# Kernel tuning notes

Hardware: AMD Instinct MI355X
Metric: run time of the kernel (lower is better)

The kernel has to match this reference:

```python
import jax, jax.numpy as jnp
import numpy as np

C = 32          # d_model / channels
D_STATE = 32
D_CONV = 4
EXPAND = 2
D_INNER = EXPAND * C          # 64
DT_RANK = (C + 15) // 16      # ceil(32/16) = 2
EPS = 1e-5


def _conv2d(x, w, b):
    # x: (B,C,H,W), w: (O,I,3,3), stride 1, padding 1 (torch Conv2d)
    y = jax.lax.conv_general_dilated(
        x, w, window_strides=(1, 1), padding=[(1, 1), (1, 1)],
        dimension_numbers=("NCHW", "OIHW", "NCHW"))
    return y + b[None, :, None, None]


def _silu(x):
    return x * jax.nn.sigmoid(x)


def _mamba(xs, in_proj_w, conv1d_w, conv1d_b, x_proj_w, dt_proj_w, dt_proj_b,
           A_log, Dp, out_proj_w):
    # xs: (B, L, C)
    xz = xs @ in_proj_w.T                       # (B, L, 2*D_INNER)
    xm, z = jnp.split(xz, 2, axis=-1)           # each (B, L, D_INNER)

    # causal depthwise conv1d along L (torch: padding=d_conv-1 then [..., :L])
    xc = xm.transpose(0, 2, 1)                  # (B, D_INNER, L)
    xc = jax.lax.conv_general_dilated(
        xc, conv1d_w, window_strides=(1,), padding=[(D_CONV - 1, 0)],
        dimension_numbers=("NCH", "OIH", "NCH"),
        feature_group_count=D_INNER)
    xm = _silu((xc + conv1d_b[None, :, None]).transpose(0, 2, 1))  # (B,L,D_INNER)

    x_dbl = xm @ x_proj_w.T                     # (B, L, DT_RANK + 2*D_STATE)
    dt = x_dbl[..., :DT_RANK]
    Bm = x_dbl[..., DT_RANK:DT_RANK + D_STATE]  # (B, L, N)
    Cm = x_dbl[..., DT_RANK + D_STATE:]         # (B, L, N)

    delta = jax.nn.softplus(dt @ dt_proj_w.T + dt_proj_b)  # (B, L, D_INNER)
    A = -jnp.exp(A_log)                                     # (D_INNER, N)

    deltaA = jnp.exp(delta[..., None] * A)                           # (B,L,D,N)
    deltaBx = delta[..., None] * Bm[:, :, None, :] * xm[..., None]   # (B,L,D,N)

    def combine(c1, c2):
        a1, b1 = c1
        a2, b2 = c2
        return a1 * a2, a2 * b1 + b2

    # parallel linear recurrence h_t = deltaA_t * h_{t-1} + deltaBx_t
    _, hstate = jax.lax.associative_scan(combine, (deltaA, deltaBx), axis=1)

    y = jnp.einsum("bldn,bln->bld", hstate, Cm) + xm * Dp
    y = y * _silu(z)
    return y @ out_proj_w.T                     # (B, L, C)


def setup_inputs() -> dict:
    key = jax.random.key(0)
    ks = jax.random.split(key, 16)
    s = 0.02
    inp = {
        "x": jax.random.normal(ks[0], (4, C, 64, 64), dtype=jnp.float32),
        "conv1_w": jax.random.normal(ks[1], (2 * C, C, 3, 3), jnp.float32) * s,
        "conv1_b": jnp.zeros((2 * C,), jnp.float32),
        "conv2_w": jax.random.normal(ks[2], (C, 2 * C, 3, 3), jnp.float32) * s,
        "conv2_b": jnp.zeros((C,), jnp.float32),
        "ln_g": jnp.ones((C,), jnp.float32),
        "ln_b": jnp.zeros((C,), jnp.float32),
        "in_proj_w": jax.random.normal(ks[3], (2 * D_INNER, C), jnp.float32) * s,
        "conv1d_w": jax.random.normal(ks[4], (D_INNER, 1, D_CONV), jnp.float32) * 0.1,
        "conv1d_b": jnp.zeros((D_INNER,), jnp.float32),
        "x_proj_w": jax.random.normal(ks[5], (DT_RANK + 2 * D_STATE, D_INNER), jnp.float32) * s,
        "dt_proj_w": jax.random.normal(ks[6], (D_INNER, DT_RANK), jnp.float32) * 0.1,
        "dt_proj_b": jax.random.normal(ks[7], (D_INNER,), jnp.float32) * 0.1 - 4.0,
        "A_log": jnp.log(jnp.tile(jnp.arange(1, D_STATE + 1, dtype=jnp.float32), (D_INNER, 1))),
        "Dp": jnp.ones((D_INNER,), jnp.float32),
        "out_proj_w": jax.random.normal(ks[8], (C, D_INNER), jnp.float32) * s,
        "smooth_w": jax.random.normal(ks[9], (C, C, 3, 3), jnp.float32) * s,
        "smooth_b": jnp.zeros((C,), jnp.float32),
    }
    return inp


def reference(x, conv1_w, conv1_b, conv2_w, conv2_b, ln_g, ln_b,
              in_proj_w, conv1d_w, conv1d_b, x_proj_w, dt_proj_w, dt_proj_b,
              A_log, Dp, out_proj_w, smooth_w, smooth_b):
    b, c, h, w = x.shape
    # convb residual
    t = jax.nn.relu(_conv2d(x, conv1_w, conv1_b))
    x = _conv2d(t, conv2_w, conv2_b) + x
    # reshape (b,c,h,w) -> (b, h*w, c) row-major (faithful to torch .reshape)
    xs = x.reshape(b, -1, c)
    # LayerNorm over last dim
    mu = jnp.mean(xs, axis=-1, keepdims=True)
    var = jnp.mean(jnp.square(xs - mu), axis=-1, keepdims=True)
    xs = (xs - mu) * jax.lax.rsqrt(var + EPS) * ln_g + ln_b
    # Mamba block
    y = _mamba(xs, in_proj_w, conv1d_w, conv1d_b, x_proj_w, dt_proj_w,
               dt_proj_b, A_log, Dp, out_proj_w)
    y = y.transpose(0, 2, 1).reshape(b, c, h, w)
    return _conv2d(y, smooth_w, smooth_b)
```

## Files before the change

### kernel.cpp

```cpp
#include <hip/hip_runtime.h>
#include <math.h>

#define SEQL 4096
#define L2E 1.44269504088896340736f

#if defined(__has_builtin)
#if __has_builtin(__builtin_amdgcn_exp2f)
#define FAST_EXP2(x) __builtin_amdgcn_exp2f(x)
#endif
#endif
#ifndef FAST_EXP2
#define FAST_EXP2(x) exp2f(x)
#endif

__device__ __forceinline__ float sigmoid_f(float x){ return 1.0f/(1.0f+expf(-x)); }

template<int CI, int CO, int COG, bool RELU, bool RES>
__global__ __launch_bounds__(256) void conv3x3_k(const float* __restrict__ in,
    const float* __restrict__ wgt, const float* __restrict__ bias,
    const float* __restrict__ res, float* __restrict__ out)
{
  constexpr int CIT = CI/4;
  __shared__ float tin[4][2][6][72];
  __shared__ float red[3][4][COG][66];
  const int tid  = threadIdx.x;
  const int lane = tid & 63;
  const int ty   = tid >> 6;
  const int h0   = blockIdx.x * 4;
  const int co0  = blockIdx.y * COG;
  const int b    = blockIdx.z;

  if (lane < 24){
    int cl = lane / 12, rem = lane % 12, r = rem >> 1, side = rem & 1;
    tin[ty][cl][r][side ? 68 : 3] = 0.0f;
  }

  float acc[4][COG];
  #pragma unroll
  for (int rr=0;rr<4;++rr)
    #pragma unroll
    for (int u=0;u<COG;++u) acc[rr][u] = 0.0f;

  const int ci0 = ty*CIT;
  for (int cig = ci0; cig < ci0 + CIT; cig += 2){
    #pragma unroll
    for (int k=0;k<3;++k){
      int idx4 = lane + (k<<6);
      int row  = idx4 >> 4;
      int cl = row/6, r = row - cl*6;
      int w4 = (idx4 & 15) << 2;
      int h  = h0 - 1 + r;
      float4 v = make_float4(0.f,0.f,0.f,0.f);
      if (h>=0 && h<64)
        v = *(const float4*)(in + ((size_t)(b*CI+cig+cl)*64 + h)*64 + w4);
      *(float4*)&tin[ty][cl][r][4+w4] = v;
    }
    #pragma unroll
    for (int cl=0; cl<2; ++cl){
      float rv[6][3];
      #pragma unroll
      for (int r=0;r<6;++r)
        #pragma unroll
        for (int c=0;c<3;++c)
          rv[r][c] = tin[ty][cl][r][3+lane+c];
      #pragma unroll
      for (int u=0;u<COG;++u){
        const float* wp = wgt + ((size_t)(co0+u)*CI + cig + cl)*9;
        #pragma unroll
        for (int rr=0;rr<4;++rr)
          #pragma unroll
          for (int j=0;j<3;++j){
            acc[rr][u] = fmaf(rv[rr+j][0], wp[3*j+0], acc[rr][u]);
            acc[rr][u] = fmaf(rv[rr+j][1], wp[3*j+1], acc[rr][u]);
            acc[rr][u] = fmaf(rv[rr+j][2], wp[3*j+2], acc[rr][u]);
          }
      }
    }
  }
  if (ty > 0){
    #pragma unroll
    for (int rr=0;rr<4;++rr)
      #pragma unroll
      for (int u=0;u<COG;++u) red[ty-1][rr][u][lane] = acc[rr][u];
  }
  __syncthreads();
  if (ty == 0){
    #pragma unroll
    for (int rr=0;rr<4;++rr)
      #pragma unroll
      for (int u=0;u<COG;++u){
        float s = acc[rr][u] + red[0][rr][u][lane] + red[1][rr][u][lane]
                + red[2][rr][u][lane] + bias[co0+u];
        size_t ob = ((size_t)(b*CO+co0+u)*64 + h0+rr)*64 + lane;
        if constexpr (RES)  s += res[ob];
        if constexpr (RELU) s = fmaxf(s, 0.0f);
        out[ob] = s;
      }
  }
}

__global__ __launch_bounds__(512) void mamba_in_k(const float* __restrict__ x2,
    const float* __restrict__ g, const float* __restrict__ be,
    const float* __restrict__ Wip, const float* __restrict__ cw,
    const float* __restrict__ cb, const float* __restrict__ Wxp,
    const float* __restrict__ Wdt, const float* __restrict__ bdt,
    const float* __restrict__ A_log,
    float* __restrict__ xm2, float* __restrict__ szb, float* __restrict__ dlt,
    float* __restrict__ Bm, float* __restrict__ Cm,
    float* __restrict__ cA, float* __restrict__ cH)
{
  __shared__ float xn[68][37];
  __shared__ float xm[64][68];
  __shared__ float xt[64][67];
  __shared__ float xd[64][67];
  const int tid = threadIdx.x, lane = tid & 63, ty = tid >> 6;
  const int bi = blockIdx.x >> 6;
  const int l0 = (blockIdx.x & 63) << 6;

  if (ty < 2){
    int t = ty*64 + lane;
    if (t < 67){
      int tok = l0 - 3 + t;
      if (tok >= 0){
        const float* row = x2 + (size_t)bi*131072 + (size_t)tok*32;
        float v[32];
        #pragma unroll
        for (int c=0;c<32;c+=4){
          float4 f = *(const float4*)(row + c);
          v[c]=f.x; v[c+1]=f.y; v[c+2]=f.z; v[c+3]=f.w;
        }
        float p[8];
        #pragma unroll
        for (int j2=0;j2<8;++j2) p[j2]=v[j2];
        #pragma unroll
        for (int i=8;i<32;i+=8){
          #pragma unroll
          for (int j2=0;j2<8;++j2) p[j2]+=v[i+j2];
        }
        float mu = (((p[0]+p[1])+(p[2]+p[3]))+((p[4]+p[5])+(p[6]+p[7]))) * 0.03125f;
        float q[8];
        #pragma unroll
        for (int j2=0;j2<8;++j2){ float dd=v[j2]-mu; q[j2]=dd*dd; }
        #pragma unroll
        for (int i=8;i<32;i+=8){
          #pragma unroll
          for (int j2=0;j2<8;++j2){ float dd=v[i+j2]-mu; q[j2]+=dd*dd; }
        }
        float var = (((q[0]+q[1])+(q[2]+q[3]))+((q[4]+q[5])+(q[6]+q[7]))) * 0.03125f;
        float rstd = 1.0f / sqrtf(var + 1e-5f);
        #pragma unroll
        for (int c=0;c<32;++c) xn[t][c] = (v[c]-mu)*rstd*g[c] + be[c];
      } else {
        #pragma unroll
        for (int c=0;c<32;++c) xn[t][c] = 0.0f;
      }
    }
  }
  __syncthreads();

  const int d0 = ty*8;
  {
    float xvA[32];
    #pragma unroll
    for (int c=0;c<32;++c) xvA[c] = xn[lane][c];
    #pragma unroll
    for (int jj=0;jj<8;++jj){
      const float* wr = Wip + (d0+jj)*32;
      float a = 0.0f;
      #pragma unroll
      for (int c=0;c<32;++c) a = fmaf(xvA[c], wr[c], a);
      xm[d0+jj][lane] = a;
    }
  }
  if (lane < 3){
    float xvB[32];
    #pragma unroll
    for (int c=0;c<32;++c) xvB[c] = xn[64+lane][c];
    #pragma unroll
    for (int jj=0;jj<8;++jj){
      const float* wr = Wip + (d0+jj)*32;
      float a = 0.0f;
      #pragma unroll
      for (int c=0;c<32;++c) a = fmaf(xvB[c], wr[c], a);
      xm[d0+jj][64+lane] = a;
    }
  }
  {
    float xvC[32];
    #pragma unroll
    for (int c=0;c<32;++c) xvC[c] = xn[lane+3][c];
    #pragma unroll
    for (int jj=0;jj<8;++jj){
      const float* wr = Wip + (64+d0+jj)*32;
      float a = 0.0f;
      #pragma unroll
      for (int c=0;c<32;++c) a = fmaf(xvC[c], wr[c], a);
      szb[((size_t)(bi*64+d0+jj))*SEQL + l0 + lane] = a * sigmoid_f(a);
    }
  }
  __syncthreads();

  #pragma unroll
  for (int jj=0;jj<8;++jj){
    int d = d0 + jj;
    float a = xm[d][lane]*cw[d*4] + xm[d][lane+1]*cw[d*4+1]
            + xm[d][lane+2]*cw[d*4+2] + xm[d][lane+3]*cw[d*4+3] + cb[d];
    float s = a * sigmoid_f(a);
    xt[lane][d] = s;
    xm2[((size_t)(bi*64+d))*SEQL + l0 + lane] = s;
  }
  __syncthreads();

  {
    float xv[64];
    #pragma unroll
    for (int c=0;c<64;++c) xv[c] = xt[lane][c];
    for (int j=ty; j<66; j+=8){
      const float* wr = Wxp + j*64;
      float a = 0.0f;
      #pragma unroll
      for (int c=0;c<64;++c) a = fmaf(xv[c], wr[c], a);
      xd[lane][j] = a;
    }
  }
  __syncthreads();

  {
    float dt0 = xd[lane][0], dt1 = xd[lane][1];
    #pragma unroll
    for (int k=0;k<8;++k){
      int d2 = ty*8 + k;
      float v = dt0*Wdt[d2*2] + dt1*Wdt[d2*2+1] + bdt[d2];
      float sp = fmaxf(v,0.0f) + log1pf(expf(-fabsf(v)));
      dlt[((size_t)(bi*64+d2))*SEQL + l0 + lane] = sp;
      xm[d2][lane] = sp;
    }
    const int which = ty >> 2, gq = ty & 3;
    float* dst = which ? Cm : Bm;
    size_t base = ((size_t)bi*SEQL + l0 + lane)*32 + gq*8;
    const int s0 = 2 + which*32 + gq*8;
    float4 f0, f1;
    f0.x = xd[lane][s0+0]; f0.y = xd[lane][s0+1]; f0.z = xd[lane][s0+2]; f0.w = xd[lane][s0+3];
    f1.x = xd[lane][s0+4]; f1.y = xd[lane][s0+5]; f1.z = xd[lane][s0+6]; f1.w = xd[lane][s0+7];
    *(float4*)(dst + base)     = f0;
    *(float4*)(dst + base + 4) = f1;
  }
  __syncthreads();

  {
    const int d  = tid >> 3;
    const int gg = tid & 7;
    const int chunk = blockIdx.x & 63;
    const int bd = bi*64 + d;
    float Av2[4], h[4] = {0,0,0,0}, aP[4] = {1,1,1,1};
    #pragma unroll
    for (int j=0;j<4;++j) Av2[j] = -expf(A_log[d*32 + gg + 8*j]) * L2E;
    #pragma unroll 4
    for (int t=0;t<64;++t){
      float dlv = xm[d][t];
      float xv2 = xt[t][d];
      #pragma unroll
      for (int j=0;j<4;++j){
        float bv = xd[t][2 + gg + 8*j];
        float a = FAST_EXP2(dlv*Av2[j]);
        h[j] = fmaf(a, h[j], dlv*bv*xv2);
        aP[j] *= a;
      }
    }
    #pragma unroll
    for (int j=0;j<4;++j){
      size_t idx = (((size_t)bd<<5) + gg + 8*j)*64 + chunk;
      cA[idx] = aP[j]; cH[idx] = h[j];
    }
  }
}

__global__ __launch_bounds__(256) void scan_p2(const float* __restrict__ dlt,
    const float* __restrict__ xssm, const float* __restrict__ Bm,
    const float* __restrict__ Cm, const float* __restrict__ A_log,
    const float* __restrict__ Dp, const float* __restrict__ sz,
    const float* __restrict__ cA, const float* __restrict__ cHs,
    float* __restrict__ yt)
{
  __shared__ float pre[32][9];
  const int tid = threadIdx.x;
  const int n = tid & 31;
  const int grp = blockIdx.x & 7;
  const int chunk = grp*8 + (tid >> 5);
  const int bd = blockIdx.x >> 3;
  const int b = bd >> 6, d = bd & 63;
  const int l0 = chunk << 6;

  if (tid < 32){
    const float* pa = cA  + (((size_t)bd<<5)+tid)*64;
    const float* ph = cHs + (((size_t)bd<<5)+tid)*64;
    float hrun = 0.0f;
    for (int c=0;c<grp*8;c+=4){
      float4 a4 = *(const float4*)(pa+c);
      float4 h4 = *(const float4*)(ph+c);
      hrun = fmaf(a4.x,hrun,h4.x);
      hrun = fmaf(a4.y,hrun,h4.y);
      hrun = fmaf(a4.z,hrun,h4.z);
      hrun = fmaf(a4.w,hrun,h4.w);
    }
    int c = grp*8;
    float4 a4 = *(const float4*)(pa+c);
    float4 h4 = *(const float4*)(ph+c);
    pre[tid][0]=hrun; hrun=fmaf(a4.x,hrun,h4.x);
    pre[tid][1]=hrun; hrun=fmaf(a4.y,hrun,h4.y);
    pre[tid][2]=hrun; hrun=fmaf(a4.z,hrun,h4.z);
    pre[tid][3]=hrun; hrun=fmaf(a4.w,hrun,h4.w);
    a4 = *(const float4*)(pa+c+4);
    h4 = *(const float4*)(ph+c+4);
    pre[tid][4]=hrun; hrun=fmaf(a4.x,hrun,h4.x);
    pre[tid][5]=hrun; hrun=fmaf(a4.y,hrun,h4.y);
    pre[tid][6]=hrun; hrun=fmaf(a4.z,hrun,h4.z);
    pre[tid][7]=hrun;
  }
  __syncthreads();

  const float Av2 = -expf(A_log[d*32+n]) * L2E;
  const float Dv = Dp[d];
  const float* del = dlt  + (size_t)bd*SEQL + l0;
  const float* xp  = xssm + (size_t)bd*SEQL + l0;
  const float* szp = sz   + (size_t)bd*SEQL + l0;
  const float* Bp  = Bm + ((size_t)b*SEQL + l0)*32 + n;
  const float* Cp  = Cm + ((size_t)b*SEQL + l0)*32 + n;
  float* yp = yt + (size_t)bd*SEQL + l0;
  float h = pre[n][tid >> 5];
  #pragma unroll 2
  for (int i0=0;i0<64;i0+=4){
    float4 d4 = *(const float4*)(del+i0);
    float4 x4 = *(const float4*)(xp +i0);
    float4 s4 = *(const float4*)(szp+i0);
    float b0 = Bp[(i0+0)*32], b1 = Bp[(i0+1)*32], b2 = Bp[(i0+2)*32], b3 = Bp[(i0+3)*32];
    float c0 = Cp[(i0+0)*32], c1 = Cp[(i0+1)*32], c2 = Cp[(i0+2)*32], c3 = Cp[(i0+3)*32];
    float a0 = FAST_EXP2(d4.x*Av2); h = fmaf(a0,h, d4.x*b0*x4.x);
    float v0 = h*c0;
    float a1 = FAST_EXP2(d4.y*Av2); h = fmaf(a1,h, d4.y*b1*x4.y);
    float v1 = h*c1;
    float a2 = FAST_EXP2(d4.z*Av2); h = fmaf(a2,h, d4.z*b2*x4.z);
    float v2 = h*c2;
    float a3 = FAST_EXP2(d4.w*Av2); h = fmaf(a3,h, d4.w*b3*x4.w);
    float v3 = h*c3;
    v0 += __shfl_xor(v0,16); v0 += __shfl_xor(v0,8); v0 += __shfl_xor(v0,4);
    v0 += __shfl_xor(v0,2);  v0 += __shfl_xor(v0,1);
    v1 += __shfl_xor(v1,16); v1 += __shfl_xor(v1,8); v1 += __shfl_xor(v1,4);
    v1 += __shfl_xor(v1,2);  v1 += __shfl_xor(v1,1);
    v2 += __shfl_xor(v2,16); v2 += __shfl_xor(v2,8); v2 += __shfl_xor(v2,4);
    v2 += __shfl_xor(v2,2);  v2 += __shfl_xor(v2,1);
    v3 += __shfl_xor(v3,16); v3 += __shfl_xor(v3,8); v3 += __shfl_xor(v3,4);
    v3 += __shfl_xor(v3,2);  v3 += __shfl_xor(v3,1);
    if (n==0){
      yp[i0+0] = fmaf(x4.x, Dv, v0) * s4.x;
      yp[i0+1] = fmaf(x4.y, Dv, v1) * s4.y;
      yp[i0+2] = fmaf(x4.z, Dv, v2) * s4.z;
      yp[i0+3] = fmaf(x4.w, Dv, v3) * s4.w;
    }
  }
}

__global__ __launch_bounds__(512) void outproj_k(const float* __restrict__ yt,
    const float* __restrict__ Wout, float* __restrict__ ym)
{
  __shared__ float ys[64][67];
  const int tid = threadIdx.x, lane = tid & 63, ty = tid >> 6;
  const int bi = blockIdx.x >> 6;
  const int l0 = (blockIdx.x & 63) << 6;
  for (int r=ty; r<64; r+=8)
    ys[lane][r] = yt[((size_t)(bi*64+r))*SEQL + l0 + lane];
  __syncthreads();
  float yv[64];
  #pragma unroll
  for (int c=0;c<64;++c) yv[c] = ys[lane][c];
  #pragma unroll
  for (int jj=0;jj<4;++jj){
    int j = ty*4 + jj;
    const float* wr = Wout + j*64;
    float acc = 0.0f;
    #pragma unroll
    for (int c=0;c<64;++c) acc = fmaf(yv[c], wr[c], acc);
    ym[((size_t)(bi*32+j))*SEQL + l0 + lane] = acc;
  }
}

extern "C" void kernel_launch(void* const* d_in, const int* in_sizes, int n_in,
                              void* d_out, int out_size, void* d_ws, size_t ws_size,
                              hipStream_t stream) {
  const float* x        = (const float*)d_in[0];
  const float* conv1_w  = (const float*)d_in[1];
  const float* conv1_b  = (const float*)d_in[2];
  const float* conv2_w  = (const float*)d_in[3];
  const float* conv2_b  = (const float*)d_in[4];
  const float* ln_g     = (const float*)d_in[5];
  const float* ln_b     = (const float*)d_in[6];
  const float* in_proj_w= (const float*)d_in[7];
  const float* conv1d_w = (const float*)d_in[8];
  const float* conv1d_b = (const float*)d_in[9];
  const float* x_proj_w = (const float*)d_in[10];
  const float* dt_proj_w= (const float*)d_in[11];
  const float* dt_proj_b= (const float*)d_in[12];
  const float* A_log    = (const float*)d_in[13];
  const float* Dp       = (const float*)d_in[14];
  const float* out_proj_w=(const float*)d_in[15];
  const float* smooth_w = (const float*)d_in[16];
  const float* smooth_b = (const float*)d_in[17];
  float* out = (float*)d_out;

  float* ws = (float*)d_ws;
  float* t      = ws;
  float* x2     = t      + 1048576;
  float* xm2    = x2     + 524288;
  float* szb    = xm2    + 1048576;
  float* dlt    = szb    + 1048576;
  float* Bmat   = dlt    + 1048576;
  float* Cmat   = Bmat   + 524288;
  float* yt     = Cmat   + 524288;
  float* ym     = yt     + 1048576;
  float* cA     = t;
  float* cH     = t + 524288;

  conv3x3_k<32,64,4,true ,false><<<dim3(16,16,4), 256, 0, stream>>>(x,  conv1_w, conv1_b, nullptr, t);
  conv3x3_k<64,32,4,false,true ><<<dim3(16,8,4), 256, 0, stream>>>(t,  conv2_w, conv2_b, x,       x2);
  mamba_in_k  <<<256, 512, 0, stream>>>(x2, ln_g, ln_b, in_proj_w, conv1d_w, conv1d_b,
                                        x_proj_w, dt_proj_w, dt_proj_b, A_log,
                                        xm2, szb, dlt, Bmat, Cmat, cA, cH);
  scan_p2     <<<2048, 256, 0, stream>>>(dlt, xm2, Bmat, Cmat, A_log, Dp, szb, cA, cH, yt);
  outproj_k   <<<256, 512, 0, stream>>>(yt, out_proj_w, ym);
  conv3x3_k<32,32,4,false,false><<<dim3(16,8,4), 256, 0, stream>>>(ym, smooth_w, smooth_b, nullptr, out);
}
```

Before: 223.0 us.

## Halve scan chunk length to 32 tokens and double block counts

The Mamba input kernel and the second scan pass now work on 32-token chunks instead of 64. That doubles the grid sizes to 512 and 4096 blocks, shortens each thread's serial recurrence, and reworks the thread-to-work mapping to fit. Chunk carry buffers move to a separate workspace region with 128 chunks per state. The intent is more parallelism and less per-thread serial latency, at the cost of a longer carry prefix in scan_p2, more halo recompute, and larger carry arrays.

After: 234.8 us. 5.3% more time.

```diff
diff --git a/kernel.cpp b/kernel.cpp
--- a/kernel.cpp
+++ b/kernel.cpp
@@ -109,154 +109,142 @@
     float* __restrict__ Bm, float* __restrict__ Cm,
     float* __restrict__ cA, float* __restrict__ cH)
 {
-  __shared__ float xn[68][37];
-  __shared__ float xm[64][68];
-  __shared__ float xt[64][67];
-  __shared__ float xd[64][67];
-  const int tid = threadIdx.x, lane = tid & 63, ty = tid >> 6;
-  const int bi = blockIdx.x >> 6;
-  const int l0 = (blockIdx.x & 63) << 6;
-
-  if (ty < 2){
-    int t = ty*64 + lane;
-    if (t < 67){
-      int tok = l0 - 3 + t;
-      if (tok >= 0){
-        const float* row = x2 + (size_t)bi*131072 + (size_t)tok*32;
-        float v[32];
+  __shared__ float xn[35][37];
+  __shared__ float xm[64][36];
+  __shared__ float xt[32][67];
+  __shared__ float xd[32][67];
+  const int tid = threadIdx.x;
+  const int bi = blockIdx.x >> 7;
+  const int chunk = blockIdx.x & 127;
+  const int l0 = chunk << 5;
+
+  if (tid < 35){
+    int tok = l0 - 3 + tid;
+    if (tok >= 0){
+      const float* row = x2 + (size_t)bi*131072 + (size_t)tok*32;
+      float v[32];
+      #pragma unroll
+      for (int c=0;c<32;c+=4){
+        float4 f = *(const float4*)(row + c);
+        v[c]=f.x; v[c+1]=f.y; v[c+2]=f.z; v[c+3]=f.w;
+      }
+      float p[8];
+      #pragma unroll
+      for (int j2=0;j2<8;++j2) p[j2]=v[j2];
+      #pragma unroll
+      for (int i=8;i<32;i+=8){
         #pragma unroll
-        for (int c=0;c<32;c+=4){
-          float4 f = *(const float4*)(row + c);
-          v[c]=f.x; v[c+1]=f.y; v[c+2]=f.z; v[c+3]=f.w;
-        }
-        float p[8];
+        for (int j2=0;j2<8;++j2) p[j2]+=v[i+j2];
+      }
+      float mu = (((p[0]+p[1])+(p[2]+p[3]))+((p[4]+p[5])+(p[6]+p[7]))) * 0.03125f;
+      float q[8];
+      #pragma unroll
+      for (int j2=0;j2<8;++j2){ float dd=v[j2]-mu; q[j2]=dd*dd; }
+      #pragma unroll
+      for (int i=8;i<32;i+=8){
         #pragma unroll
-        for (int j2=0;j2<8;++j2) p[j2]=v[j2];
-        #pragma unroll
-        for (int i=8;i<32;i+=8){
-          #pragma unroll
-          for (int j2=0;j2<8;++j2) p[j2]+=v[i+j2];
-        }
-        float mu = (((p[0]+p[1])+(p[2]+p[3]))+((p[4]+p[5])+(p[6]+p[7]))) * 0.03125f;
-        float q[8];
-        #pragma unroll
-        for (int j2=0;j2<8;++j2){ float dd=v[j2]-mu; q[j2]=dd*dd; }
-        #pragma unroll
-        for (int i=8;i<32;i+=8){
-          #pragma unroll
-          for (int j2=0;j2<8;++j2){ float dd=v[i+j2]-mu; q[j2]+=dd*dd; }
-        }
-        float var = (((q[0]+q[1])+(q[2]+q[3]))+((q[4]+q[5])+(q[6]+q[7]))) * 0.03125f;
-        float rstd = 1.0f / sqrtf(var + 1e-5f);
-        #pragma unroll
-        for (int c=0;c<32;++c) xn[t][c] = (v[c]-mu)*rstd*g[c] + be[c];
-      } else {
-        #pragma unroll
-        for (int c=0;c<32;++c) xn[t][c] = 0.0f;
-      }
-    }
-  }
-  __syncthreads();
-
-  const int d0 = ty*8;
+        for (int j2=0;j2<8;++j2){ float dd=v[i+j2]-mu; q[j2]+=dd*dd; }
+      }
+      float var = (((q[0]+q[1])+(q[2]+q[3]))+((q[4]+q[5])+(q[6]+q[7]))) * 0.03125f;
+      float rstd = 1.0f / sqrtf(var + 1e-5f);
+      #pragma unroll
+      for (int c=0;c<32;++c) xn[tid][c] = (v[c]-mu)*rstd*g[c] + be[c];
+    } else {
+      #pragma unroll
+      for (int c=0;c<32;++c) xn[tid][c] = 0.0f;
+    }
+  }
+  __syncthreads();
+
   {
-    float xvA[32];
-    #pragma unroll
-    for (int c=0;c<32;++c) xvA[c] = xn[lane][c];
-    #pragma unroll
-    for (int jj=0;jj<8;++jj){
-      const float* wr = Wip + (d0+jj)*32;
+    const int t = tid & 31, jg = tid >> 5;
+    float xv[32];
+    #pragma unroll
+    for (int c=0;c<32;++c) xv[c] = xn[t+3][c];
+    #pragma unroll
+    for (int k=0;k<8;++k){
+      int j = jg*8 + k;
+      const float* wr = Wip + j*32;
       float a = 0.0f;
       #pragma unroll
-      for (int c=0;c<32;++c) a = fmaf(xvA[c], wr[c], a);
-      xm[d0+jj][lane] = a;
-    }
-  }
-  if (lane < 3){
-    float xvB[32];
-    #pragma unroll
-    for (int c=0;c<32;++c) xvB[c] = xn[64+lane][c];
-    #pragma unroll
-    for (int jj=0;jj<8;++jj){
-      const float* wr = Wip + (d0+jj)*32;
-      float a = 0.0f;
-      #pragma unroll
-      for (int c=0;c<32;++c) a = fmaf(xvB[c], wr[c], a);
-      xm[d0+jj][64+lane] = a;
-    }
-  }
+      for (int c=0;c<32;++c) a = fmaf(xv[c], wr[c], a);
+      if (j < 64) xm[j][t+3] = a;
+      else        szb[((size_t)(bi*64 + (j-64)))*SEQL + l0 + t] = a * sigmoid_f(a);
+    }
+  }
+  if (tid < 192){
+    int t = tid % 3, j = tid / 3;
+    float xv[32];
+    #pragma unroll
+    for (int c=0;c<32;++c) xv[c] = xn[t][c];
+    const float* wr = Wip + j*32;
+    float a = 0.0f;
+    #pragma unroll
+    for (int c=0;c<32;++c) a = fmaf(xv[c], wr[c], a);
+    xm[j][t] = a;
+  }
+  __syncthreads();
+
   {
-    float xvC[32];
-    #pragma unroll
-    for (int c=0;c<32;++c) xvC[c] = xn[lane+3][c];
-    #pragma unroll
-    for (int jj=0;jj<8;++jj){
-      const float* wr = Wip + (64+d0+jj)*32;
-      float a = 0.0f;
-      #pragma unroll
-      for (int c=0;c<32;++c) a = fmaf(xvC[c], wr[c], a);
-      szb[((size_t)(bi*64+d0+jj))*SEQL + l0 + lane] = a * sigmoid_f(a);
-    }
-  }
-  __syncthreads();
-
-  #pragma unroll
-  for (int jj=0;jj<8;++jj){
-    int d = d0 + jj;
-    float a = xm[d][lane]*cw[d*4] + xm[d][lane+1]*cw[d*4+1]
-            + xm[d][lane+2]*cw[d*4+2] + xm[d][lane+3]*cw[d*4+3] + cb[d];
-    float s = a * sigmoid_f(a);
-    xt[lane][d] = s;
-    xm2[((size_t)(bi*64+d))*SEQL + l0 + lane] = s;
+    const int d = tid >> 3, t0 = (tid & 7) << 2;
+    const float w0=cw[d*4], w1=cw[d*4+1], w2=cw[d*4+2], w3=cw[d*4+3], bv=cb[d];
+    float r[4];
+    #pragma unroll
+    for (int k=0;k<4;++k){
+      int t = t0 + k;
+      float a = xm[d][t]*w0 + xm[d][t+1]*w1 + xm[d][t+2]*w2 + xm[d][t+3]*w3 + bv;
+      float s = a * sigmoid_f(a);
+      xt[t][d] = s;
+      r[k] = s;
+    }
+    *(float4*)(xm2 + ((size_t)(bi*64+d))*SEQL + l0 + t0) = make_float4(r[0],r[1],r[2],r[3]);
   }
   __syncthreads();
 
   {
+    const int tok = tid & 31, jg = tid >> 5;
     float xv[64];
     #pragma unroll
-    for (int c=0;c<64;++c) xv[c] = xt[lane][c];
-    for (int j=ty; j<66; j+=8){
+    for (int c=0;c<64;++c) xv[c] = xt[tok][c];
+    for (int j=jg; j<66; j+=16){
       const float* wr = Wxp + j*64;
       float a = 0.0f;
       #pragma unroll
       for (int c=0;c<64;++c) a = fmaf(xv[c], wr[c], a);
-      xd[lane][j] = a;
+      xd[tok][j] = a;
     }
   }
   __syncthreads();
 
   {
-    float dt0 = xd[lane][0], dt1 = xd[lane][1];
-    #pragma unroll
-    for (int k=0;k<8;++k){
-      int d2 = ty*8 + k;
+    const int tok = tid & 31, gg = tid >> 5;
+    float dt0 = xd[tok][0], dt1 = xd[tok][1];
+    #pragma unroll
+    for (int k=0;k<4;++k){
+      int d2 = gg*4 + k;
       float v = dt0*Wdt[d2*2] + dt1*Wdt[d2*2+1] + bdt[d2];
       float sp = fmaxf(v,0.0f) + log1pf(expf(-fabsf(v)));
-      dlt[((size_t)(bi*64+d2))*SEQL + l0 + lane] = sp;
-      xm[d2][lane] = sp;
-    }
-    const int which = ty >> 2, gq = ty & 3;
+      dlt[((size_t)(bi*64+d2))*SEQL + l0 + tok] = sp;
+      xm[d2][tok] = sp;
+    }
+    const int which = gg >> 3, n0 = (gg & 7)*4;
     float* dst = which ? Cm : Bm;
-    size_t base = ((size_t)bi*SEQL + l0 + lane)*32 + gq*8;
-    const int s0 = 2 + which*32 + gq*8;
-    float4 f0, f1;
-    f0.x = xd[lane][s0+0]; f0.y = xd[lane][s0+1]; f0.z = xd[lane][s0+2]; f0.w = xd[lane][s0+3];
-    f1.x = xd[lane][s0+4]; f1.y = xd[lane][s0+5]; f1.z = xd[lane][s0+6]; f1.w = xd[lane][s0+7];
-    *(float4*)(dst + base)     = f0;
-    *(float4*)(dst + base + 4) = f1;
+    const int s0 = 2 + which*32 + n0;
+    float4 f;
+    f.x = xd[tok][s0]; f.y = xd[tok][s0+1]; f.z = xd[tok][s0+2]; f.w = xd[tok][s0+3];
+    *(float4*)(dst + ((size_t)bi*SEQL + l0 + tok)*32 + n0) = f;
   }
   __syncthreads();
 
   {
     const int d  = tid >> 3;
     const int gg = tid & 7;
-    const int chunk = blockIdx.x & 63;
     const int bd = bi*64 + d;
     float Av2[4], h[4] = {0,0,0,0}, aP[4] = {1,1,1,1};
     #pragma unroll
     for (int j=0;j<4;++j) Av2[j] = -expf(A_log[d*32 + gg + 8*j]) * L2E;
     #pragma unroll 4
-    for (int t=0;t<64;++t){
+    for (int t=0;t<32;++t){
       float dlv = xm[d][t];
       float xv2 = xt[t][d];
       #pragma unroll
@@ -269,7 +257,7 @@
     }
     #pragma unroll
     for (int j=0;j<4;++j){
-      size_t idx = (((size_t)bd<<5) + gg + 8*j)*64 + chunk;
+      size_t idx = (((size_t)bd<<5) + gg + 8*j)*128 + chunk;
       cA[idx] = aP[j]; cH[idx] = h[j];
     }
   }
@@ -285,15 +273,15 @@
   __shared__ float pre[32][9];
   const int tid = threadIdx.x;
   const int n = tid & 31;
-  const int grp = blockIdx.x & 7;
+  const int grp = blockIdx.x & 15;
   const int chunk = grp*8 + (tid >> 5);
-  const int bd = blockIdx.x >> 3;
+  const int bd = blockIdx.x >> 4;
   const int b = bd >> 6, d = bd & 63;
-  const int l0 = chunk << 6;
+  const int l0 = chunk << 5;
 
   if (tid < 32){
-    const float* pa = cA  + (((size_t)bd<<5)+tid)*64;
-    const float* ph = cHs + (((size_t)bd<<5)+tid)*64;
+    const float* pa = cA  + (((size_t)bd<<5)+tid)*128;
+    const float* ph = cHs + (((size_t)bd<<5)+tid)*128;
     float hrun = 0.0f;
     for (int c=0;c<grp*8;c+=4){
       float4 a4 = *(const float4*)(pa+c);
@@ -329,7 +317,7 @@
   float* yp = yt + (size_t)bd*SEQL + l0;
   float h = pre[n][tid >> 5];
   #pragma unroll 2
-  for (int i0=0;i0<64;i0+=4){
+  for (int i0=0;i0<32;i0+=4){
     float4 d4 = *(const float4*)(del+i0);
     float4 x4 = *(const float4*)(xp +i0);
     float4 s4 = *(const float4*)(szp+i0);
@@ -417,15 +405,15 @@
   float* Cmat   = Bmat   + 524288;
   float* yt     = Cmat   + 524288;
   float* ym     = yt     + 1048576;
-  float* cA     = t;
-  float* cH     = t + 524288;
+  float* cA     = ym     + 524288;
+  float* cH     = cA     + 1048576;
 
   conv3x3_k<32,64,4,true ,false><<<dim3(16,16,4), 256, 0, stream>>>(x,  conv1_w, conv1_b, nullptr, t);
   conv3x3_k<64,32,4,false,true ><<<dim3(16,8,4), 256, 0, stream>>>(t,  conv2_w, conv2_b, x,       x2);
-  mamba_in_k  <<<256, 512, 0, stream>>>(x2, ln_g, ln_b, in_proj_w, conv1d_w, conv1d_b,
+  mamba_in_k  <<<512, 512, 0, stream>>>(x2, ln_g, ln_b, in_proj_w, conv1d_w, conv1d_b,
                                         x_proj_w, dt_proj_w, dt_proj_b, A_log,
                                         xm2, szb, dlt, Bmat, Cmat, cA, cH);
-  scan_p2     <<<2048, 256, 0, stream>>>(dlt, xm2, Bmat, Cmat, A_log, Dp, szb, cA, cH, yt);
+  scan_p2     <<<4096, 256, 0, stream>>>(dlt, xm2, Bmat, Cmat, A_log, Dp, szb, cA, cH, yt);
   outproj_k   <<<256, 512, 0, stream>>>(yt, out_proj_w, ym);
   conv3x3_k<32,32,4,false,false><<<dim3(16,8,4), 256, 0, stream>>>(ym, smooth_w, smooth_b, nullptr, out);
 }
```

## Give each scan thread four states and interleave the B/C layout for float4 loads

Applied to the files above, without the earlier changes.

The second scan pass now has each thread own four state indices (n = gg + 8j) for one chunk instead of one state per lane. This replaces the five-step 32-lane shuffle reduction with a three-step 8-lane reduction plus local FMAs. mamba_in_k writes B and C in an interleaved order so each thread fetches its four state values with one float4 load per timestep, and y is stored as a float4. The grid shrinks from 2048 to 512 blocks, each covering 32 chunks, which means more serial per-thread work and less parallelism across blocks.

Result: faster. 205.4 us (median of 2 runs) (-7.9%).

```diff
diff --git a/kernel.cpp b/kernel.cpp
--- a/kernel.cpp
+++ b/kernel.cpp
@@ -238,10 +238,13 @@
     const int which = ty >> 2, gq = ty & 3;
     float* dst = which ? Cm : Bm;
     size_t base = ((size_t)bi*SEQL + l0 + lane)*32 + gq*8;
-    const int s0 = 2 + which*32 + gq*8;
+    const int s2 = 2 + which*32;
+    const int q0 = gq*2;
     float4 f0, f1;
-    f0.x = xd[lane][s0+0]; f0.y = xd[lane][s0+1]; f0.z = xd[lane][s0+2]; f0.w = xd[lane][s0+3];
-    f1.x = xd[lane][s0+4]; f1.y = xd[lane][s0+5]; f1.z = xd[lane][s0+6]; f1.w = xd[lane][s0+7];
+    f0.x = xd[lane][s2+q0+ 0]; f0.y = xd[lane][s2+q0+ 8];
+    f0.z = xd[lane][s2+q0+16]; f0.w = xd[lane][s2+q0+24];
+    f1.x = xd[lane][s2+q0+ 1]; f1.y = xd[lane][s2+q0+ 9];
+    f1.z = xd[lane][s2+q0+17]; f1.w = xd[lane][s2+q0+25];
     *(float4*)(dst + base)     = f0;
     *(float4*)(dst + base + 4) = f1;
   }
@@ -282,81 +285,80 @@
     const float* __restrict__ cA, const float* __restrict__ cHs,
     float* __restrict__ yt)
 {
-  __shared__ float pre[32][9];
+  __shared__ float pre[32][34];
   const int tid = threadIdx.x;
-  const int n = tid & 31;
-  const int grp = blockIdx.x & 7;
-  const int chunk = grp*8 + (tid >> 5);
-  const int bd = blockIdx.x >> 3;
+  const int grp = blockIdx.x & 1;
+  const int bd  = blockIdx.x >> 1;
   const int b = bd >> 6, d = bd & 63;
-  const int l0 = chunk << 6;
+  const int c0 = grp << 5;
 
   if (tid < 32){
     const float* pa = cA  + (((size_t)bd<<5)+tid)*64;
     const float* ph = cHs + (((size_t)bd<<5)+tid)*64;
     float hrun = 0.0f;
-    for (int c=0;c<grp*8;c+=4){
-      float4 a4 = *(const float4*)(pa+c);
-      float4 h4 = *(const float4*)(ph+c);
-      hrun = fmaf(a4.x,hrun,h4.x);
-      hrun = fmaf(a4.y,hrun,h4.y);
-      hrun = fmaf(a4.z,hrun,h4.z);
-      hrun = fmaf(a4.w,hrun,h4.w);
-    }
-    int c = grp*8;
-    float4 a4 = *(const float4*)(pa+c);
-    float4 h4 = *(const float4*)(ph+c);
-    pre[tid][0]=hrun; hrun=fmaf(a4.x,hrun,h4.x);
-    pre[tid][1]=hrun; hrun=fmaf(a4.y,hrun,h4.y);
-    pre[tid][2]=hrun; hrun=fmaf(a4.z,hrun,h4.z);
-    pre[tid][3]=hrun; hrun=fmaf(a4.w,hrun,h4.w);
-    a4 = *(const float4*)(pa+c+4);
-    h4 = *(const float4*)(ph+c+4);
-    pre[tid][4]=hrun; hrun=fmaf(a4.x,hrun,h4.x);
-    pre[tid][5]=hrun; hrun=fmaf(a4.y,hrun,h4.y);
-    pre[tid][6]=hrun; hrun=fmaf(a4.z,hrun,h4.z);
-    pre[tid][7]=hrun;
-  }
-  __syncthreads();
-
-  const float Av2 = -expf(A_log[d*32+n]) * L2E;
+    if (grp){
+      #pragma unroll 4
+      for (int c=0;c<32;c+=4){
+        float4 a4 = *(const float4*)(pa+c);
+        float4 h4 = *(const float4*)(ph+c);
+        hrun = fmaf(a4.x,hrun,h4.x);
+        hrun = fmaf(a4.y,hrun,h4.y);
+        hrun = fmaf(a4.z,hrun,h4.z);
+        hrun = fmaf(a4.w,hrun,h4.w);
+      }
+    }
+    #pragma unroll 4
+    for (int k=0;k<32;k+=4){
+      float4 a4 = *(const float4*)(pa+c0+k);
+      float4 h4 = *(const float4*)(ph+c0+k);
+      pre[tid][k+0]=hrun; hrun=fmaf(a4.x,hrun,h4.x);
+      pre[tid][k+1]=hrun; hrun=fmaf(a4.y,hrun,h4.y);
+      pre[tid][k+2]=hrun; hrun=fmaf(a4.z,hrun,h4.z);
+      pre[tid][k+3]=hrun; hrun=fmaf(a4.w,hrun,h4.w);
+    }
+  }
+  __syncthreads();
+
+  const int lc = tid >> 3, gg = tid & 7;
+  const int chunk = c0 + lc;
+  const int l0 = chunk << 6;
   const float Dv = Dp[d];
+  float Av2[4], h[4];
+  #pragma unroll
+  for (int j=0;j<4;++j){
+    Av2[j] = -expf(A_log[d*32 + gg + 8*j]) * L2E;
+    h[j] = pre[gg + 8*j][lc];
+  }
   const float* del = dlt  + (size_t)bd*SEQL + l0;
   const float* xp  = xssm + (size_t)bd*SEQL + l0;
   const float* szp = sz   + (size_t)bd*SEQL + l0;
-  const float* Bp  = Bm + ((size_t)b*SEQL + l0)*32 + n;
-  const float* Cp  = Cm + ((size_t)b*SEQL + l0)*32 + n;
+  const float* Bp  = Bm + ((size_t)b*SEQL + l0)*32 + gg*4;
+  const float* Cp  = Cm + ((size_t)b*SEQL + l0)*32 + gg*4;
   float* yp = yt + (size_t)bd*SEQL + l0;
-  float h = pre[n][tid >> 5];
+
   #pragma unroll 2
   for (int i0=0;i0<64;i0+=4){
     float4 d4 = *(const float4*)(del+i0);
     float4 x4 = *(const float4*)(xp +i0);
     float4 s4 = *(const float4*)(szp+i0);
-    float b0 = Bp[(i0+0)*32], b1 = Bp[(i0+1)*32], b2 = Bp[(i0+2)*32], b3 = Bp[(i0+3)*32];
-    float c0 = Cp[(i0+0)*32], c1 = Cp[(i0+1)*32], c2 = Cp[(i0+2)*32], c3 = Cp[(i0+3)*32];
-    float a0 = FAST_EXP2(d4.x*Av2); h = fmaf(a0,h, d4.x*b0*x4.x);
-    float v0 = h*c0;
-    float a1 = FAST_EXP2(d4.y*Av2); h = fmaf(a1,h, d4.y*b1*x4.y);
-    float v1 = h*c1;
-    float a2 = FAST_EXP2(d4.z*Av2); h = fmaf(a2,h, d4.z*b2*x4.z);
-    float v2 = h*c2;
-    float a3 = FAST_EXP2(d4.w*Av2); h = fmaf(a3,h, d4.w*b3*x4.w);
-    float v3 = h*c3;
-    v0 += __shfl_xor(v0,16); v0 += __shfl_xor(v0,8); v0 += __shfl_xor(v0,4);
-    v0 += __shfl_xor(v0,2);  v0 += __shfl_xor(v0,1);
-    v1 += __shfl_xor(v1,16); v1 += __shfl_xor(v1,8); v1 += __shfl_xor(v1,4);
-    v1 += __shfl_xor(v1,2);  v1 += __shfl_xor(v1,1);
-    v2 += __shfl_xor(v2,16); v2 += __shfl_xor(v2,8); v2 += __shfl_xor(v2,4);
-    v2 += __shfl_xor(v2,2);  v2 += __shfl_xor(v2,1);
-    v3 += __shfl_xor(v3,16); v3 += __shfl_xor(v3,8); v3 += __shfl_xor(v3,4);
-    v3 += __shfl_xor(v3,2);  v3 += __shfl_xor(v3,1);
-    if (n==0){
-      yp[i0+0] = fmaf(x4.x, Dv, v0) * s4.x;
-      yp[i0+1] = fmaf(x4.y, Dv, v1) * s4.y;
-      yp[i0+2] = fmaf(x4.z, Dv, v2) * s4.z;
-      yp[i0+3] = fmaf(x4.w, Dv, v3) * s4.w;
-    }
+    float y[4];
+    #pragma unroll
+    for (int t=0;t<4;++t){
+      float dl = (t==0)? d4.x : (t==1)? d4.y : (t==2)? d4.z : d4.w;
+      float xl = (t==0)? x4.x : (t==1)? x4.y : (t==2)? x4.z : x4.w;
+      float sl = (t==0)? s4.x : (t==1)? s4.y : (t==2)? s4.z : s4.w;
+      float4 bv = *(const float4*)(Bp + (i0+t)*32);
+      float4 cv = *(const float4*)(Cp + (i0+t)*32);
+      float a0 = FAST_EXP2(dl*Av2[0]); h[0] = fmaf(a0, h[0], dl*bv.x*xl);
+      float a1 = FAST_EXP2(dl*Av2[1]); h[1] = fmaf(a1, h[1], dl*bv.y*xl);
+      float a2 = FAST_EXP2(dl*Av2[2]); h[2] = fmaf(a2, h[2], dl*bv.z*xl);
+      float a3 = FAST_EXP2(dl*Av2[3]); h[3] = fmaf(a3, h[3], dl*bv.w*xl);
+      float v = fmaf(h[3], cv.w, fmaf(h[2], cv.z, fmaf(h[1], cv.y, h[0]*cv.x)));
+      v += __shfl_xor(v,1); v += __shfl_xor(v,2); v += __shfl_xor(v,4);
+      y[t] = fmaf(xl, Dv, v) * sl;
+    }
+    if (gg == 0)
+      *(float4*)(yp + i0) = make_float4(y[0], y[1], y[2], y[3]);
   }
 }
 
@@ -425,7 +427,7 @@
   mamba_in_k  <<<256, 512, 0, stream>>>(x2, ln_g, ln_b, in_proj_w, conv1d_w, conv1d_b,
                                         x_proj_w, dt_proj_w, dt_proj_b, A_log,
                                         xm2, szb, dlt, Bmat, Cmat, cA, cH);
-  scan_p2     <<<2048, 256, 0, stream>>>(dlt, xm2, Bmat, Cmat, A_log, Dp, szb, cA, cH, yt);
+  scan_p2     <<<512, 256, 0, stream>>>(dlt, xm2, Bmat, Cmat, A_log, Dp, szb, cA, cH, yt);
   outproj_k   <<<256, 512, 0, stream>>>(yt, out_proj_w, ym);
   conv3x3_k<32,32,4,false,false><<<dim3(16,8,4), 256, 0, stream>>>(ym, smooth_w, smooth_b, nullptr, out);
 }
```
